# Performance work log

Hardware: AMD Instinct MI355X
Metric: run time of the kernel (lower is better)

The kernel has to match this reference:

```python
import jax, jax.numpy as jnp
import numpy as np

N_NODES = 20000
N_EDGES = 200000
NUM_GRAPHS = 512
IN_C = 16      # in_channel
P1 = 128       # edge MLP hidden
P2 = 16        # base channel width
F_E = 16       # nbr_edge_features
C1_OUT = 3 * P2  # 48
C2_OUT = 2 * P2  # 32
C3_OUT = P2      # 16


def _nnconv(x, src, tgt, ea, W1, b1, W2, b2, root, bias, in_c, out_c):
    # edge MLP -> per-edge weight matrix [E, in_c, out_c]
    h = jax.nn.relu(ea @ W1 + b1)
    We = (h @ W2 + b2).reshape(-1, in_c, out_c)
    msg = jnp.einsum('ei,eio->eo', x[src], We)          # gather + batched matmul
    n = x.shape[0]
    agg = jax.ops.segment_sum(msg, tgt, num_segments=n)  # scatter
    deg = jax.ops.segment_sum(jnp.ones((src.shape[0],), x.dtype), tgt, num_segments=n)
    agg = agg / jnp.maximum(deg, 1.0)[:, None]           # aggr='mean'
    return agg + x @ root + bias


def _set2set(x, batch, Wih, Whh, bih, bhh, num_graphs, steps=2):
    H = x.shape[-1]
    q_star = jnp.zeros((num_graphs, 2 * H), x.dtype)
    h = jnp.zeros((num_graphs, H), x.dtype)
    c = jnp.zeros_like(h)
    for _ in range(steps):
        gates = q_star @ Wih.T + bih + h @ Whh.T + bhh   # LSTM cell (i,f,g,o)
        i, f, g, o = jnp.split(gates, 4, axis=-1)
        c = jax.nn.sigmoid(f) * c + jax.nn.sigmoid(i) * jnp.tanh(g)
        h = jax.nn.sigmoid(o) * jnp.tanh(c)
        e = jnp.sum(x * h[batch], axis=-1)               # attention logits per node
        emax = jax.ops.segment_max(e, batch, num_segments=num_graphs)
        a = jnp.exp(e - jnp.maximum(emax, -1e30)[batch])
        asum = jax.ops.segment_sum(a, batch, num_segments=num_graphs)
        a = a / jnp.maximum(asum, 1e-16)[batch]
        r = jax.ops.segment_sum(a[:, None] * x, batch, num_segments=num_graphs)
        q_star = jnp.concatenate([h, r], axis=-1)
    return q_star


def setup_inputs() -> dict:
    key = jax.random.key(0)
    ks = iter(jax.random.split(key, 40))
    d = {}
    d['x'] = jax.random.normal(next(ks), (N_NODES, IN_C), jnp.float32)
    d['edge_index'] = jax.random.randint(next(ks), (2, N_EDGES), 0, N_NODES)
    d['edge_attr'] = jax.random.uniform(next(ks), (N_EDGES, F_E), jnp.float32)
    d['batch'] = jnp.sort(jax.random.randint(next(ks), (N_NODES,), 0, NUM_GRAPHS))

    def lin(ki, fan_in, fan_out):
        s = 1.0 / np.sqrt(fan_in)
        return jax.random.uniform(ki, (fan_in, fan_out), jnp.float32, -s, s)

    for name, ic, oc in [('c1', IN_C, C1_OUT), ('c2', C1_OUT, C2_OUT), ('c3', C2_OUT, C3_OUT)]:
        d[name + '_W1'] = lin(next(ks), F_E, P1)
        d[name + '_b1'] = jnp.zeros((P1,), jnp.float32)
        d[name + '_W2'] = lin(next(ks), P1, ic * oc) * 0.1
        d[name + '_b2'] = jnp.zeros((ic * oc,), jnp.float32)
        d[name + '_root'] = lin(next(ks), ic, oc)
        d[name + '_bias'] = jnp.zeros((oc,), jnp.float32)

    H = P2
    s = 1.0 / np.sqrt(H)
    d['lstm_Wih'] = jax.random.uniform(next(ks), (4 * H, 2 * H), jnp.float32, -s, s)
    d['lstm_Whh'] = jax.random.uniform(next(ks), (4 * H, H), jnp.float32, -s, s)
    d['lstm_bih'] = jnp.zeros((4 * H,), jnp.float32)
    d['lstm_bhh'] = jnp.zeros((4 * H,), jnp.float32)

    tot = 2 * P2
    d['lin1_W'] = lin(next(ks), tot, tot // 2)
    d['lin1_b'] = jnp.zeros((tot // 2,), jnp.float32)
    d['lin2_W'] = lin(next(ks), tot // 2, tot // 4)
    d['lin2_b'] = jnp.zeros((tot // 4,), jnp.float32)
    d['linf_W'] = lin(next(ks), tot // 4, 1)
    d['linf_b'] = jnp.zeros((1,), jnp.float32)
    return d


def reference(x, edge_index, edge_attr, batch,
              c1_W1, c1_b1, c1_W2, c1_b2, c1_root, c1_bias,
              c2_W1, c2_b1, c2_W2, c2_b2, c2_root, c2_bias,
              c3_W1, c3_b1, c3_W2, c3_b2, c3_root, c3_bias,
              lstm_Wih, lstm_Whh, lstm_bih, lstm_bhh,
              lin1_W, lin1_b, lin2_W, lin2_b, linf_W, linf_b):
    src, tgt = edge_index[0], edge_index[1]
    y = jax.nn.relu(_nnconv(x, src, tgt, edge_attr, c1_W1, c1_b1, c1_W2, c1_b2, c1_root, c1_bias, IN_C, C1_OUT))
    y = jax.nn.relu(_nnconv(y, src, tgt, edge_attr, c2_W1, c2_b1, c2_W2, c2_b2, c2_root, c2_bias, C1_OUT, C2_OUT))
    y = jax.nn.relu(_nnconv(y, src, tgt, edge_attr, c3_W1, c3_b1, c3_W2, c3_b2, c3_root, c3_bias, C2_OUT, C3_OUT))
    y = _set2set(y, batch, lstm_Wih, lstm_Whh, lstm_bih, lstm_bhh, NUM_GRAPHS, steps=2)  # [B, 2*P2]
    y = jax.nn.relu(y @ lin1_W + lin1_b)
    y = jax.nn.relu(y @ lin2_W + lin2_b)
    y = (y @ linf_W + linf_b).squeeze(-1)  # [B]
    return y
```

## Files before the change

### kernel.cpp

```cpp
#include <hip/hip_runtime.h>

#define NN 20000
#define NE 200000
#define NG 512

typedef float v2f __attribute__((ext_vector_type(2)));

__device__ __forceinline__ int lowerb(const int* a, int n, int v){
  int lo=0, hi=n;
  while(lo<hi){ int m=(lo+hi)>>1; if(a[m]<v) lo=m+1; else hi=m; }
  return lo;
}

template<int AUX>
__device__ __forceinline__ void gload_lds16(const float4* g, float4* l){
  __builtin_amdgcn_global_load_lds(
    (const __attribute__((address_space(1))) void*)(g),
    (__attribute__((address_space(3))) void*)(l), 16, 0, AUX);
}

__global__ void k_count(const int* __restrict__ tgt, int* __restrict__ cnt){
  int e = blockIdx.x*blockDim.x + threadIdx.x;
  if(e<NE) atomicAdd(&cnt[tgt[e]], 1);
}

__global__ void k_scan(const int* __restrict__ cnt, int* __restrict__ row_start){
  __shared__ int part[1024];
  int t = threadIdx.x;
  const int CH = (NN + 1023)/1024;
  int i0 = t*CH;
  int s = 0;
  for(int j=0;j<CH;j++){ int i=i0+j; if(i<NN) s += cnt[i]; }
  part[t] = s; __syncthreads();
  for(int d=1; d<1024; d<<=1){
    int v = (t>=d) ? part[t-d] : 0;
    __syncthreads();
    part[t] += v;
    __syncthreads();
  }
  int run = (t==0) ? 0 : part[t-1];
  for(int j=0;j<CH;j++){ int i=i0+j; if(i<NN){ row_start[i]=run; run += cnt[i]; } }
  if(t==0) row_start[NN] = part[1023];
}

__global__ void k_place(const int* __restrict__ src, const int* __restrict__ tgt,
                        const float* __restrict__ ea,
                        const int* __restrict__ row_start, int* __restrict__ cur,
                        int* __restrict__ es_src, float* __restrict__ es_ea){
  int e = blockIdx.x*blockDim.x + threadIdx.x;
  if(e>=NE) return;
  int n = tgt[e];
  int pos = row_start[n] + atomicAdd(&cur[n],1);
  es_src[pos] = src[e];
  const float4* s = (const float4*)ea + (size_t)e*4;
  float4* d = (float4*)es_ea + (size_t)pos*4;
  d[0]=s[0]; d[1]=s[1]; d[2]=s[2]; d[3]=s[3];
}

__launch_bounds__(256, 4)
__global__ void k_hmlp(const float* __restrict__ es_ea, const float* __restrict__ W1,
                       const float* __restrict__ b1, float* __restrict__ H){
  const int pc = threadIdx.x & 31, er = threadIdx.x >> 5;
  v2f w1a[16], w1b[16];
  #pragma unroll
  for(int i=0;i<16;i++){
    float4 w = *(const float4*)&W1[i*128 + pc*4];
    w1a[i] = v2f{w.x, w.y};
    w1b[i] = v2f{w.z, w.w};
  }
  const float4 bv = *(const float4*)&b1[pc*4];
  for(size_t e0 = (size_t)blockIdx.x*8; e0 < NE; e0 += (size_t)gridDim.x*8){
    const size_t e = e0 + er;
    v2f h01 = v2f{bv.x, bv.y}, h23 = v2f{bv.z, bv.w};
    float eav[16];
    const float4* eap = (const float4*)(es_ea + e*16);
    #pragma unroll
    for(int q=0;q<4;q++){
      float4 v = eap[q];
      eav[q*4+0]=v.x; eav[q*4+1]=v.y; eav[q*4+2]=v.z; eav[q*4+3]=v.w;
    }
    #pragma unroll
    for(int i=0;i<16;i++){
      v2f e2 = v2f{eav[i], eav[i]};
      h01 += e2*w1a[i];
      h23 += e2*w1b[i];
    }
    float4 hv;
    hv.x = fmaxf(h01[0],0.f); hv.y = fmaxf(h01[1],0.f);
    hv.z = fmaxf(h23[0],0.f); hv.w = fmaxf(h23[1],0.f);
    *(float4*)&H[e*128 + pc*4] = hv;
  }
}

template<int IC>
__global__ void k_xbar(const float* __restrict__ x, const int* __restrict__ es_src,
                       const int* __restrict__ row_start, float* __restrict__ xbar){
  constexpr int TI = IC/16;
  const int wid = threadIdx.x>>6, lane = threadIdx.x&63;
  const int eg = lane>>4, ig = lane&15;
  for(int n0 = blockIdx.x*4; n0 < NN; n0 += gridDim.x*4){
    const int n = n0 + wid;
    const int a = row_start[n], b = row_start[n+1];
    float s[TI];
    #pragma unroll
    for(int u=0;u<TI;u++) s[u]=0.f;
    for(int e=a+eg; e<b; e+=4){
      int sn = es_src[e];
      #pragma unroll
      for(int u=0;u<TI;u++) s[u] += x[(size_t)sn*IC + ig*TI + u];
    }
    #pragma unroll
    for(int u=0;u<TI;u++){
      s[u] += __shfl_xor(s[u], 16, 64);
      s[u] += __shfl_xor(s[u], 32, 64);
    }
    if(eg==0){
      float dinv = 1.f/fmaxf((float)(b-a), 1.f);
      #pragma unroll
      for(int u=0;u<TI;u++) xbar[(size_t)n*IC + ig*TI + u] = s[u]*dinv;
    }
  }
}

template<int IC, int OC, int PLEN, int KS, int BN, int PP, int TI, int OQ, int TO, bool PF, int EB>
__launch_bounds__(256, 3)
__global__ void k_layer(const float* __restrict__ x_in, const float* __restrict__ H,
                        const int* __restrict__ es_src, const int* __restrict__ row_start,
                        const float* __restrict__ W2, float* __restrict__ part)
{
  constexpr int K    = PLEN*IC;
  constexpr int HV4  = PLEN/4;
  constexpr int XV   = IC/4;
  constexpr int NIW  = IC/TI;
  constexpr int NPW  = PLEN/PP;
  constexpr int G    = BN/4;
  constexpr int KQL  = 64/OQ;
  constexpr int TSPL = 4*KQL;
  constexpr int J    = (K/4)/TSPL;
  constexpr int NH4  = (EB*HV4 + 255)/256;
  constexpr int NX4  = (EB*XV  + 255)/256;
  constexpr int TI2  = TI/2;
  constexpr int NP   = TO/2;
  constexpr bool TODD = (TO & 1);
  static_assert(TI%2==0, "packed scatter needs even TI");
  static_assert(NPW*NIW==64, "wave tile covers 64 lanes");
  static_assert(G*PP*TI <= 48, "spill-safe accumulator");
  static_assert(EB*(PLEN+IC) <= BN*K, "staging alias fits in S");
  static_assert((EB*HV4)%256==0, "hb tail must not round into xs region");
  static_assert(EB*PLEN/4 + NX4*256 <= BN*K/4, "xs tail rounding stays inside S");
  static_assert(OQ*TO==OC && (K/4)%TSPL==0, "gemm tiling");
  static_assert(J%2==0, "ping-pong needs even J");

  __shared__ __align__(16) float S[BN*K];
  __shared__ int rs_s[BN+1], ro[BN+1];

  float* hb = S;
  float* xs = S + EB*PLEN;

  const int tid = threadIdx.x;
  const int wid = tid>>6, lane = tid&63;
  const int split = blockIdx.x % KS;
  const int nb = blockIdx.x / KS;
  const int n0 = nb*BN;
  const int p04 = split*HV4;

  if(tid<=BN) rs_s[tid] = row_start[n0+tid];
  __syncthreads();
  const int estart = rs_s[0], eend = rs_s[BN];

  const int pw = lane / NIW;
  const int iw = lane - pw*NIW;

  v2f acc2[G][PP][TI2];
  #pragma unroll
  for(int g=0;g<G;g++)
    #pragma unroll
    for(int p=0;p<PP;p++)
      #pragma unroll
      for(int u=0;u<TI2;u++) acc2[g][p][u]=v2f{0.f,0.f};

  const float4* H4 = (const float4*)H;
  const float4* x4 = (const float4*)x_in;

  for(int bstart=estart; bstart<eend; bstart+=EB){
    const int ebc = min(EB, eend-bstart);
    if(tid<=BN){ int v = rs_s[tid]-bstart; ro[tid] = min(max(v,0), ebc); }
    const int hb_lim = ebc*HV4, xs_lim = ebc*XV;
    int sn_r[NX4];
    #pragma unroll
    for(int c=0;c<NX4;c++){
      int jc = min(tid + c*256, xs_lim-1);
      sn_r[c] = es_src[bstart + jc/XV];
    }
    #pragma unroll
    for(int c=0;c<NH4;c++){
      int j = tid + c*256;
      int jc = min(j, hb_lim-1);
      int e = jc/HV4, q = jc - e*HV4;
      gload_lds16<2>(H4 + (size_t)(bstart+e)*32 + p04 + q, ((float4*)hb) + j);
    }
    #pragma unroll
    for(int c=0;c<NX4;c++){
      int j = tid + c*256;
      int jc = min(j, xs_lim-1);
      int q = jc - (jc/XV)*XV;
      gload_lds16<0>(x4 + (size_t)sn_r[c]*XV + q, ((float4*)xs) + j);
    }
    __syncthreads();
    if constexpr (PF){
      #pragma unroll
      for(int g=0; g<G; g++){
        const int nl = wid*G + g;
        const int a = ro[nl], b = ro[nl+1];
        if(a>=b) continue;
        float hv[PP]; v2f xv2[TI2];
        #pragma unroll
        for(int p=0;p<PP;p++) hv[p] = hb[a*PLEN + pw*PP + p];
        #pragma unroll
        for(int u=0;u<TI2;u++) xv2[u] = *(const v2f*)&xs[a*IC + iw*TI + 2*u];
        for(int e=a; e<b; e++){
          float hn[PP]; v2f xn2[TI2];
          if(e+1<b){
            #pragma unroll
            for(int p=0;p<PP;p++) hn[p] = hb[(e+1)*PLEN + pw*PP + p];
            #pragma unroll
            for(int u=0;u<TI2;u++) xn2[u] = *(const v2f*)&xs[(e+1)*IC + iw*TI + 2*u];
          }
          #pragma unroll
          for(int p=0;p<PP;p++){
            v2f h2 = v2f{hv[p], hv[p]};
            #pragma unroll
            for(int u=0;u<TI2;u++) acc2[g][p][u] += h2*xv2[u];
          }
          #pragma unroll
          for(int p=0;p<PP;p++) hv[p]=hn[p];
          #pragma unroll
          for(int u=0;u<TI2;u++) xv2[u]=xn2[u];
        }
      }
    } else {
      #pragma unroll
      for(int g=0; g<G; g++){
        const int nl = wid*G + g;
        const int a = ro[nl], b = ro[nl+1];
        for(int e=a; e<b; e++){
          float hv[PP];
          #pragma unroll
          for(int p=0;p<PP;p++) hv[p] = hb[e*PLEN + pw*PP + p];
          v2f xv2[TI2];
          #pragma unroll
          for(int u=0;u<TI2;u++) xv2[u] = *(const v2f*)&xs[e*IC + iw*TI + 2*u];
          #pragma unroll
          for(int p=0;p<PP;p++){
            v2f h2 = v2f{hv[p], hv[p]};
            #pragma unroll
            for(int u=0;u<TI2;u++) acc2[g][p][u] += h2*xv2[u];
          }
        }
      }
    }
    __syncthreads();
  }

  #pragma unroll
  for(int g=0; g<G; g++){
    const int nl = wid*G + g;
    const float dv = 1.f/fmaxf((float)(rs_s[nl+1]-rs_s[nl]), 1.f);
    const v2f dv2 = v2f{dv, dv};
    #pragma unroll
    for(int p=0;p<PP;p++)
      #pragma unroll
      for(int u=0;u<TI2;u++)
        *(v2f*)&S[(nl*PLEN + pw*PP + p)*IC + iw*TI + 2*u] = acc2[g][p][u]*dv2;
  }

  const int oq  = lane % OQ;
  const int kql = lane / OQ;
  const int o0  = oq*TO;
  const float* W2b = W2 + (size_t)split*K*OC + o0;

  auto LOADW = [&](int j, v2f (&wv2)[4][NP], float (&wvs)[4]){
    const int k4 = j*TSPL + wid*KQL + kql;
    #pragma unroll
    for(int r=0;r<4;r++){
      const float* wr = W2b + (size_t)(4*k4+r)*OC;
      if constexpr (TO==4){
        float4 a=*(const float4*)wr;
        wv2[r][0]=v2f{a.x,a.y}; wv2[r][1]=v2f{a.z,a.w};
      } else if constexpr (TO==3){
        wv2[r][0]=v2f{wr[0],wr[1]}; wvs[r]=wr[2];
      } else {
        float2 a=*(const float2*)wr;
        wv2[r][0]=v2f{a.x,a.y};
      }
    }
  };

  v2f outp2[BN][NP];
  float outs[BN];
  #pragma unroll
  for(int n=0;n<BN;n++){
    #pragma unroll
    for(int t=0;t<NP;t++) outp2[n][t]=v2f{0.f,0.f};
    outs[n]=0.f;
  }

  v2f wvA[4][NP], wvB[4][NP];
  float wsA[4], wsB[4];
  LOADW(0, wvA, wsA);
  __syncthreads();

  #pragma unroll 1
  for(int j=0;j<J;j+=2){
    LOADW(j+1, wvB, wsB);
    {
      const int k4 = j*TSPL + wid*KQL + kql;
      #pragma unroll
      for(int n=0;n<BN;n++){
        float4 sv = *(const float4*)&S[n*K + 4*k4];
        v2f s0=v2f{sv.x,sv.x}, s1=v2f{sv.y,sv.y}, s2=v2f{sv.z,sv.z}, s3=v2f{sv.w,sv.w};
        #pragma unroll
        for(int t=0;t<NP;t++)
          outp2[n][t] += s0*wvA[0][t] + s1*wvA[1][t] + s2*wvA[2][t] + s3*wvA[3][t];
        if constexpr (TODD)
          outs[n] += sv.x*wsA[0] + sv.y*wsA[1] + sv.z*wsA[2] + sv.w*wsA[3];
      }
    }
    if(j+2<J) LOADW(j+2, wvA, wsA);
    {
      const int k4 = (j+1)*TSPL + wid*KQL + kql;
      #pragma unroll
      for(int n=0;n<BN;n++){
        float4 sv = *(const float4*)&S[n*K + 4*k4];
        v2f s0=v2f{sv.x,sv.x}, s1=v2f{sv.y,sv.y}, s2=v2f{sv.z,sv.z}, s3=v2f{sv.w,sv.w};
        #pragma unroll
        for(int t=0;t<NP;t++)
          outp2[n][t] += s0*wvB[0][t] + s1*wvB[1][t] + s2*wvB[2][t] + s3*wvB[3][t];
        if constexpr (TODD)
          outs[n] += sv.x*wsB[0] + sv.y*wsB[1] + sv.z*wsB[2] + sv.w*wsB[3];
      }
    }
  }

  #pragma unroll
  for(int m=OQ; m<64; m<<=1)
    #pragma unroll
    for(int n=0;n<BN;n++){
      #pragma unroll
      for(int t=0;t<NP;t++){
        outp2[n][t][0] += __shfl_xor(outp2[n][t][0], m, 64);
        outp2[n][t][1] += __shfl_xor(outp2[n][t][1], m, 64);
      }
      if constexpr (TODD) outs[n] += __shfl_xor(outs[n], m, 64);
    }

  if(kql==0){
    float* slice = part + (size_t)(split*4+wid)*NN*OC;
    #pragma unroll
    for(int n=0;n<BN;n++){
      float* dst = slice + (size_t)(n0+n)*OC + o0;
      if constexpr (TO==4){
        *(float4*)dst = make_float4(outp2[n][0][0],outp2[n][0][1],outp2[n][1][0],outp2[n][1][1]);
      } else if constexpr (TO==3){
        dst[0]=outp2[n][0][0]; dst[1]=outp2[n][0][1]; dst[2]=outs[n];
      } else {
        *(float2*)dst = make_float2(outp2[n][0][0],outp2[n][0][1]);
      }
    }
  }
}

template<int IC, int OC, int SL>
__global__ void k_epi(const float* __restrict__ part, const float* __restrict__ x,
                      const float* __restrict__ xbar,
                      const float* __restrict__ root, const float* __restrict__ b2,
                      const float* __restrict__ bias, float* __restrict__ y)
{
  for(int idx = blockIdx.x*256 + threadIdx.x; idx < NN*OC; idx += gridDim.x*256){
    int n = idx/OC, o = idx - n*OC;
    float v = bias[o];
    #pragma unroll
    for(int s=0;s<SL;s++) v += part[(size_t)s*NN*OC + idx];
    #pragma unroll
    for(int i=0;i<IC;i++) v += x[(size_t)n*IC+i]*root[i*OC+o];
    #pragma unroll
    for(int i=0;i<IC;i++) v += xbar[(size_t)n*IC+i]*b2[i*OC+o];
    y[idx] = fmaxf(v, 0.f);
  }
}

__global__ void k_s2s(const float* __restrict__ xg, const int* __restrict__ batch,
  const float* __restrict__ Wih, const float* __restrict__ Whh,
  const float* __restrict__ bih, const float* __restrict__ bhh,
  const float* __restrict__ l1W, const float* __restrict__ l1b,
  const float* __restrict__ l2W, const float* __restrict__ l2b,
  const float* __restrict__ lfW, const float* __restrict__ lfb,
  float* __restrict__ out)
{
  int g = blockIdx.x, lane = threadIdx.x;
  __shared__ float hs[16], cs[16], qs[32], gs[64], rs[16];
  int r0 = lowerb(batch, NN, g);
  int r1 = lowerb(batch, NN, g+1);
  if(lane<16){ hs[lane]=0.f; cs[lane]=0.f; }
  if(lane<32) qs[lane]=0.f;
  __syncthreads();
  for(int step=0; step<2; step++){
    float gate = bih[lane] + bhh[lane];
    for(int k=0;k<32;k++) gate += qs[k]*Wih[lane*32+k];
    for(int k=0;k<16;k++) gate += hs[k]*Whh[lane*16+k];
    gs[lane] = gate;
    __syncthreads();
    if(lane<16){
      float ig = 1.f/(1.f+expf(-gs[lane]));
      float fg = 1.f/(1.f+expf(-gs[lane+16]));
      float gg = tanhf(gs[lane+32]);
      float og = 1.f/(1.f+expf(-gs[lane+48]));
      float cn = fg*cs[lane] + ig*gg;
      cs[lane] = cn;
      hs[lane] = og*tanhf(cn);
    }
    __syncthreads();
    float m = -1e30f;
    for(int n=r0+lane; n<r1; n+=64){
      float e=0.f;
      for(int k=0;k<16;k++) e += xg[n*16+k]*hs[k];
      m = fmaxf(m, e);
    }
    for(int d=1; d<64; d<<=1) m = fmaxf(m, __shfl_xor(m, d));
    float ssum = 0.f;
    float racc[16];
    #pragma unroll
    for(int k=0;k<16;k++) racc[k]=0.f;
    for(int n=r0+lane; n<r1; n+=64){
      float e=0.f, xv[16];
      #pragma unroll
      for(int k=0;k<16;k++){ xv[k]=xg[n*16+k]; e += xv[k]*hs[k]; }
      float a = expf(e - m);
      ssum += a;
      #pragma unroll
      for(int k=0;k<16;k++) racc[k] += a*xv[k];
    }
    for(int d=1; d<64; d<<=1) ssum += __shfl_xor(ssum, d);
    #pragma unroll
    for(int k=0;k<16;k++)
      for(int d=1; d<64; d<<=1) racc[k] += __shfl_xor(racc[k], d);
    ssum = fmaxf(ssum, 1e-16f);
    if(lane==0){
      #pragma unroll
      for(int k=0;k<16;k++) rs[k] = racc[k]/ssum;
    }
    __syncthreads();
    if(lane<16){ qs[lane]=hs[lane]; qs[16+lane]=rs[lane]; }
    __syncthreads();
  }
  if(lane<16){
    float v = l1b[lane];
    for(int k=0;k<32;k++) v += qs[k]*l1W[k*16+lane];
    gs[lane] = fmaxf(v,0.f);
  }
  __syncthreads();
  if(lane<8){
    float v = l2b[lane];
    for(int k=0;k<16;k++) v += gs[k]*l2W[k*8+lane];
    gs[32+lane] = fmaxf(v,0.f);
  }
  __syncthreads();
  if(lane==0){
    float v = lfb[0];
    for(int k=0;k<8;k++) v += gs[32+k]*lfW[k];
    out[g] = v;
  }
}

extern "C" void kernel_launch(void* const* d_in, const int* in_sizes, int n_in,
                              void* d_out, int out_size, void* d_ws, size_t ws_size,
                              hipStream_t stream) {
  const float* x0   = (const float*)d_in[0];
  const int*   ei   = (const int*)d_in[1];
  const float* ea   = (const float*)d_in[2];
  const int*   batch= (const int*)d_in[3];
  const float* c1W1 = (const float*)d_in[4];  const float* c1b1 = (const float*)d_in[5];
  const float* c1W2 = (const float*)d_in[6];  const float* c1b2 = (const float*)d_in[7];
  const float* c1rt = (const float*)d_in[8];  const float* c1bs = (const float*)d_in[9];
  const float* c2W1 = (const float*)d_in[10]; const float* c2b1 = (const float*)d_in[11];
  const float* c2W2 = (const float*)d_in[12]; const float* c2b2 = (const float*)d_in[13];
  const float* c2rt = (const float*)d_in[14]; const float* c2bs = (const float*)d_in[15];
  const float* c3W1 = (const float*)d_in[16]; const float* c3b1 = (const float*)d_in[17];
  const float* c3W2 = (const float*)d_in[18]; const float* c3b2 = (const float*)d_in[19];
  const float* c3rt = (const float*)d_in[20]; const float* c3bs = (const float*)d_in[21];
  const float* Wih  = (const float*)d_in[22]; const float* Whh  = (const float*)d_in[23];
  const float* bih  = (const float*)d_in[24]; const float* bhh  = (const float*)d_in[25];
  const float* l1W  = (const float*)d_in[26]; const float* l1b  = (const float*)d_in[27];
  const float* l2W  = (const float*)d_in[28]; const float* l2b  = (const float*)d_in[29];
  const float* lfW  = (const float*)d_in[30]; const float* lfb  = (const float*)d_in[31];
  float* out = (float*)d_out;

  const int* src = ei;
  const int* tgt = ei + NE;

  char* w = (char*)d_ws;
  auto carve = [&](size_t bytes)->void*{ void* p = (void*)w; w += (bytes + 255) & ~(size_t)255; return p; };
  int*   row_start = (int*)carve((NN+1)*sizeof(int));
  int*   cur       = (int*)carve(NN*sizeof(int));
  int*   es_src    = (int*)carve(NE*sizeof(int));
  float* es_ea     = (float*)carve((size_t)NE*16*sizeof(float));
  float* Hbuf      = (float*)carve((size_t)NE*128*sizeof(float));
  float* xbar      = (float*)carve((size_t)NN*48*sizeof(float));
  float* y1   = (float*)carve((size_t)NN*48*sizeof(float));
  float* y2   = (float*)carve((size_t)NN*32*sizeof(float));
  float* y3   = (float*)carve((size_t)NN*16*sizeof(float));
  float* part = (float*)carve((size_t)16*NN*48*sizeof(float));

  hipMemsetAsync(cur, 0, NN*sizeof(int), stream);
  k_count<<<(NE+255)/256, 256, 0, stream>>>(tgt, cur);
  k_scan<<<1, 1024, 0, stream>>>(cur, row_start);
  hipMemsetAsync(cur, 0, NN*sizeof(int), stream);
  k_place<<<(NE+255)/256, 256, 0, stream>>>(src, tgt, ea, row_start, cur, es_src, es_ea);

  k_hmlp<<<2048, 256, 0, stream>>>(es_ea, c1W1, c1b1, Hbuf);
  k_xbar<16><<<2048, 256, 0, stream>>>(x0, es_src, row_start, xbar);
  k_layer<16,48,64,2,8,4,4,16,3,true,96><<<(NN/8)*2, 256, 0, stream>>>(x0, Hbuf, es_src, row_start, c1W2, part);
  k_epi<16,48,8><<<2048, 256, 0, stream>>>(part, x0, xbar, c1rt, c1b2, c1bs, y1);

  k_hmlp<<<2048, 256, 0, stream>>>(es_ea, c2W1, c2b1, Hbuf);
  k_xbar<48><<<2048, 256, 0, stream>>>(y1, es_src, row_start, xbar);
  k_layer<48,32,32,4,8,4,6,8,4,true,128><<<(NN/8)*4, 256, 0, stream>>>(y1, Hbuf, es_src, row_start, c2W2, part);
  k_epi<48,32,16><<<2048, 256, 0, stream>>>(part, y1, xbar, c2rt, c2b2, c2bs, y2);

  k_hmlp<<<2048, 256, 0, stream>>>(es_ea, c3W1, c3b1, Hbuf);
  k_xbar<32><<<2048, 256, 0, stream>>>(y2, es_src, row_start, xbar);
  k_layer<32,16,64,2,4,4,8,4,4,true,64><<<(NN/4)*2, 256, 0, stream>>>(y2, Hbuf, es_src, row_start, c3W2, part);
  k_epi<32,16,8><<<2048, 256, 0, stream>>>(part, y2, xbar, c3rt, c3b2, c3bs, y3);

  k_s2s<<<NG, 64, 0, stream>>>(y3, batch, Wih, Whh, bih, bhh, l1W, l1b, l2W, l2b, lfW, lfb, out);
}
```

Baseline: 737.0 us.

## Fuse edge-MLP hidden compute and neighbor mean into the layer kernel

Removes the separate k_hmlp and k_xbar kernels and the large per-edge hidden buffer H. Each layer block now stages raw edge attributes into shared memory and recomputes its PLEN-wide slice of the ReLU hidden layer on the fly. The mean of gathered neighbour features (xbar) is accumulated alongside the main product and written by split 0. This trades a write and read of an E×128 float buffer plus two kernel launches per layer for redundant first-layer MLP arithmetic, an extra barrier per edge batch, and more registers. Layer 1's edge batch size also shrinks from 96 to 64.

Result: no change. 723.5 us (-1.8%).

```diff
diff --git a/kernel.cpp b/kernel.cpp
--- a/kernel.cpp
+++ b/kernel.cpp
@@ -57,79 +57,15 @@
   d[0]=s[0]; d[1]=s[1]; d[2]=s[2]; d[3]=s[3];
 }
 
-__launch_bounds__(256, 4)
-__global__ void k_hmlp(const float* __restrict__ es_ea, const float* __restrict__ W1,
-                       const float* __restrict__ b1, float* __restrict__ H){
-  const int pc = threadIdx.x & 31, er = threadIdx.x >> 5;
-  v2f w1a[16], w1b[16];
-  #pragma unroll
-  for(int i=0;i<16;i++){
-    float4 w = *(const float4*)&W1[i*128 + pc*4];
-    w1a[i] = v2f{w.x, w.y};
-    w1b[i] = v2f{w.z, w.w};
-  }
-  const float4 bv = *(const float4*)&b1[pc*4];
-  for(size_t e0 = (size_t)blockIdx.x*8; e0 < NE; e0 += (size_t)gridDim.x*8){
-    const size_t e = e0 + er;
-    v2f h01 = v2f{bv.x, bv.y}, h23 = v2f{bv.z, bv.w};
-    float eav[16];
-    const float4* eap = (const float4*)(es_ea + e*16);
-    #pragma unroll
-    for(int q=0;q<4;q++){
-      float4 v = eap[q];
-      eav[q*4+0]=v.x; eav[q*4+1]=v.y; eav[q*4+2]=v.z; eav[q*4+3]=v.w;
-    }
-    #pragma unroll
-    for(int i=0;i<16;i++){
-      v2f e2 = v2f{eav[i], eav[i]};
-      h01 += e2*w1a[i];
-      h23 += e2*w1b[i];
-    }
-    float4 hv;
-    hv.x = fmaxf(h01[0],0.f); hv.y = fmaxf(h01[1],0.f);
-    hv.z = fmaxf(h23[0],0.f); hv.w = fmaxf(h23[1],0.f);
-    *(float4*)&H[e*128 + pc*4] = hv;
-  }
-}
-
-template<int IC>
-__global__ void k_xbar(const float* __restrict__ x, const int* __restrict__ es_src,
-                       const int* __restrict__ row_start, float* __restrict__ xbar){
-  constexpr int TI = IC/16;
-  const int wid = threadIdx.x>>6, lane = threadIdx.x&63;
-  const int eg = lane>>4, ig = lane&15;
-  for(int n0 = blockIdx.x*4; n0 < NN; n0 += gridDim.x*4){
-    const int n = n0 + wid;
-    const int a = row_start[n], b = row_start[n+1];
-    float s[TI];
-    #pragma unroll
-    for(int u=0;u<TI;u++) s[u]=0.f;
-    for(int e=a+eg; e<b; e+=4){
-      int sn = es_src[e];
-      #pragma unroll
-      for(int u=0;u<TI;u++) s[u] += x[(size_t)sn*IC + ig*TI + u];
-    }
-    #pragma unroll
-    for(int u=0;u<TI;u++){
-      s[u] += __shfl_xor(s[u], 16, 64);
-      s[u] += __shfl_xor(s[u], 32, 64);
-    }
-    if(eg==0){
-      float dinv = 1.f/fmaxf((float)(b-a), 1.f);
-      #pragma unroll
-      for(int u=0;u<TI;u++) xbar[(size_t)n*IC + ig*TI + u] = s[u]*dinv;
-    }
-  }
-}
-
 template<int IC, int OC, int PLEN, int KS, int BN, int PP, int TI, int OQ, int TO, bool PF, int EB>
 __launch_bounds__(256, 3)
-__global__ void k_layer(const float* __restrict__ x_in, const float* __restrict__ H,
+__global__ void k_layer(const float* __restrict__ x_in, const float* __restrict__ es_ea,
                         const int* __restrict__ es_src, const int* __restrict__ row_start,
-                        const float* __restrict__ W2, float* __restrict__ part)
+                        const float* __restrict__ W1, const float* __restrict__ b1,
+                        const float* __restrict__ W2, float* __restrict__ part,
+                        float* __restrict__ xbar_out)
 {
   constexpr int K    = PLEN*IC;
-  constexpr int HV4  = PLEN/4;
   constexpr int XV   = IC/4;
   constexpr int NIW  = IC/TI;
   constexpr int NPW  = PLEN/PP;
@@ -137,32 +73,34 @@
   constexpr int KQL  = 64/OQ;
   constexpr int TSPL = 4*KQL;
   constexpr int J    = (K/4)/TSPL;
-  constexpr int NH4  = (EB*HV4 + 255)/256;
-  constexpr int NX4  = (EB*XV  + 255)/256;
+  constexpr int NEA  = EB/64;
+  constexpr int NX4  = (EB*XV)/256;
   constexpr int TI2  = TI/2;
   constexpr int NP   = TO/2;
   constexpr bool TODD = (TO & 1);
+  constexpr int EPB  = 256/PLEN;
   static_assert(TI%2==0, "packed scatter needs even TI");
+  static_assert(256%PLEN==0, "H-compute mapping");
+  static_assert(EB%64==0, "ea region must be exact 256-f4 chunks");
+  static_assert((EB*XV)%256==0, "xs region must be exact 256-f4 chunks");
+  static_assert(EB*(PLEN+16+IC) <= BN*K, "staging alias fits in S");
   static_assert(NPW*NIW==64, "wave tile covers 64 lanes");
   static_assert(G*PP*TI <= 48, "spill-safe accumulator");
-  static_assert(EB*(PLEN+IC) <= BN*K, "staging alias fits in S");
-  static_assert((EB*HV4)%256==0, "hb tail must not round into xs region");
-  static_assert(EB*PLEN/4 + NX4*256 <= BN*K/4, "xs tail rounding stays inside S");
   static_assert(OQ*TO==OC && (K/4)%TSPL==0, "gemm tiling");
   static_assert(J%2==0, "ping-pong needs even J");
 
   __shared__ __align__(16) float S[BN*K];
   __shared__ int rs_s[BN+1], ro[BN+1];
 
-  float* hb = S;
-  float* xs = S + EB*PLEN;
+  float* hb  = S;
+  float* eas = S + EB*PLEN;
+  float* xs  = S + EB*(PLEN+16);
 
   const int tid = threadIdx.x;
   const int wid = tid>>6, lane = tid&63;
   const int split = blockIdx.x % KS;
   const int nb = blockIdx.x / KS;
   const int n0 = nb*BN;
-  const int p04 = split*HV4;
 
   if(tid<=BN) rs_s[tid] = row_start[n0+tid];
   __syncthreads();
@@ -170,22 +108,32 @@
 
   const int pw = lane / NIW;
   const int iw = lane - pw*NIW;
+  const int pcol = tid % PLEN, erow = tid / PLEN;
+
+  float w1c[16];
+  const float b1c = b1[split*PLEN + pcol];
+  #pragma unroll
+  for(int i=0;i<16;i++) w1c[i] = W1[i*128 + split*PLEN + pcol];
 
   v2f acc2[G][PP][TI2];
+  v2f xsum2[G][TI2];
   #pragma unroll
-  for(int g=0;g<G;g++)
+  for(int g=0;g<G;g++){
     #pragma unroll
     for(int p=0;p<PP;p++)
       #pragma unroll
       for(int u=0;u<TI2;u++) acc2[g][p][u]=v2f{0.f,0.f};
-
-  const float4* H4 = (const float4*)H;
-  const float4* x4 = (const float4*)x_in;
+    #pragma unroll
+    for(int u=0;u<TI2;u++) xsum2[g][u]=v2f{0.f,0.f};
+  }
+
+  const float4* EA4 = (const float4*)es_ea;
+  const float4* x4  = (const float4*)x_in;
 
   for(int bstart=estart; bstart<eend; bstart+=EB){
     const int ebc = min(EB, eend-bstart);
     if(tid<=BN){ int v = rs_s[tid]-bstart; ro[tid] = min(max(v,0), ebc); }
-    const int hb_lim = ebc*HV4, xs_lim = ebc*XV;
+    const int ea_lim = ebc*4, xs_lim = ebc*XV;
     int sn_r[NX4];
     #pragma unroll
     for(int c=0;c<NX4;c++){
@@ -193,11 +141,10 @@
       sn_r[c] = es_src[bstart + jc/XV];
     }
     #pragma unroll
-    for(int c=0;c<NH4;c++){
+    for(int c=0;c<NEA;c++){
       int j = tid + c*256;
-      int jc = min(j, hb_lim-1);
-      int e = jc/HV4, q = jc - e*HV4;
-      gload_lds16<2>(H4 + (size_t)(bstart+e)*32 + p04 + q, ((float4*)hb) + j);
+      int jc = min(j, ea_lim-1);
+      gload_lds16<0>(EA4 + (size_t)bstart*4 + jc, ((float4*)eas) + j);
     }
     #pragma unroll
     for(int c=0;c<NX4;c++){
@@ -207,6 +154,18 @@
       gload_lds16<0>(x4 + (size_t)sn_r[c]*XV + q, ((float4*)xs) + j);
     }
     __syncthreads();
+
+    for(int ec = erow; ec < ebc; ec += EPB){
+      float h = b1c;
+      #pragma unroll
+      for(int q=0;q<4;q++){
+        float4 a = *(const float4*)&eas[ec*16 + 4*q];
+        h += a.x*w1c[4*q] + a.y*w1c[4*q+1] + a.z*w1c[4*q+2] + a.w*w1c[4*q+3];
+      }
+      hb[ec*PLEN + pcol] = fmaxf(h, 0.f);
+    }
+    __syncthreads();
+
     if constexpr (PF){
       #pragma unroll
       for(int g=0; g<G; g++){
@@ -233,6 +192,8 @@
             for(int u=0;u<TI2;u++) acc2[g][p][u] += h2*xv2[u];
           }
           #pragma unroll
+          for(int u=0;u<TI2;u++) xsum2[g][u] += xv2[u];
+          #pragma unroll
           for(int p=0;p<PP;p++) hv[p]=hn[p];
           #pragma unroll
           for(int u=0;u<TI2;u++) xv2[u]=xn2[u];
@@ -256,10 +217,25 @@
             #pragma unroll
             for(int u=0;u<TI2;u++) acc2[g][p][u] += h2*xv2[u];
           }
+          #pragma unroll
+          for(int u=0;u<TI2;u++) xsum2[g][u] += xv2[u];
         }
       }
     }
     __syncthreads();
+  }
+
+  if(split==0 && pw==0){
+    #pragma unroll
+    for(int g=0;g<G;g++){
+      const int nl = wid*G + g;
+      const float dv = 1.f/fmaxf((float)(rs_s[nl+1]-rs_s[nl]), 1.f);
+      #pragma unroll
+      for(int u=0;u<TI2;u++){
+        v2f r = xsum2[g][u]*v2f{dv,dv};
+        *(v2f*)&xbar_out[(size_t)(n0+nl)*IC + iw*TI + 2*u] = r;
+      }
+    }
   }
 
   #pragma unroll
@@ -504,7 +480,6 @@
   int*   cur       = (int*)carve(NN*sizeof(int));
   int*   es_src    = (int*)carve(NE*sizeof(int));
   float* es_ea     = (float*)carve((size_t)NE*16*sizeof(float));
-  float* Hbuf      = (float*)carve((size_t)NE*128*sizeof(float));
   float* xbar      = (float*)carve((size_t)NN*48*sizeof(float));
   float* y1   = (float*)carve((size_t)NN*48*sizeof(float));
   float* y2   = (float*)carve((size_t)NN*32*sizeof(float));
@@ -517,19 +492,16 @@
   hipMemsetAsync(cur, 0, NN*sizeof(int), stream);
   k_place<<<(NE+255)/256, 256, 0, stream>>>(src, tgt, ea, row_start, cur, es_src, es_ea);
 
-  k_hmlp<<<2048, 256, 0, stream>>>(es_ea, c1W1, c1b1, Hbuf);
-  k_xbar<16><<<2048, 256, 0, stream>>>(x0, es_src, row_start, xbar);
-  k_layer<16,48,64,2,8,4,4,16,3,true,96><<<(NN/8)*2, 256, 0, stream>>>(x0, Hbuf, es_src, row_start, c1W2, part);
+  k_layer<16,48,64,2,8,4,4,16,3,true,64><<<(NN/8)*2, 256, 0, stream>>>(
+      x0, es_ea, es_src, row_start, c1W1, c1b1, c1W2, part, xbar);
   k_epi<16,48,8><<<2048, 256, 0, stream>>>(part, x0, xbar, c1rt, c1b2, c1bs, y1);
 
-  k_hmlp<<<2048, 256, 0, stream>>>(es_ea, c2W1, c2b1, Hbuf);
-  k_xbar<48><<<2048, 256, 0, stream>>>(y1, es_src, row_start, xbar);
-  k_layer<48,32,32,4,8,4,6,8,4,true,128><<<(NN/8)*4, 256, 0, stream>>>(y1, Hbuf, es_src, row_start, c2W2, part);
+  k_layer<48,32,32,4,8,4,6,8,4,true,128><<<(NN/8)*4, 256, 0, stream>>>(
+      y1, es_ea, es_src, row_start, c2W1, c2b1, c2W2, part, xbar);
   k_epi<48,32,16><<<2048, 256, 0, stream>>>(part, y1, xbar, c2rt, c2b2, c2bs, y2);
 
-  k_hmlp<<<2048, 256, 0, stream>>>(es_ea, c3W1, c3b1, Hbuf);
-  k_xbar<32><<<2048, 256, 0, stream>>>(y2, es_src, row_start, xbar);
-  k_layer<32,16,64,2,4,4,8,4,4,true,64><<<(NN/4)*2, 256, 0, stream>>>(y2, Hbuf, es_src, row_start, c3W2, part);
+  k_layer<32,16,64,2,4,4,8,4,4,true,64><<<(NN/4)*2, 256, 0, stream>>>(
+      y2, es_ea, es_src, row_start, c3W1, c3b1, c3W2, part, xbar);
   k_epi<32,16,8><<<2048, 256, 0, stream>>>(part, y2, xbar, c3rt, c3b2, c3bs, y3);
 
   k_s2s<<<NG, 64, 0, stream>>>(y3, batch, Wih, Whh, bih, bhh, l1W, l1b, l2W, l2b, lfW, lfb, out);
```
